# Performance work log

Hardware: AMD Instinct MI355X
Metric: run time of the kernel (lower is better)

The kernel has to match this reference:

```python
import jax, jax.numpy as jnp
import numpy as np

OBS = 4096      # flattened observation size (hardcoded in down_sampler)
ENC = 1024      # encoding_size
LAT = 512       # policy_latent_size
ACT = 3         # action_space_n
B = 4096        # batch
NMAX = 8        # max neighbors (padded ragged dim)


def setup_inputs() -> dict:
    key = jax.random.key(0)
    ks = jax.random.split(key, 16)

    def w(i, shape, fan_in):
        return jax.random.normal(ks[i], shape, jnp.float32) * (1.0 / np.sqrt(fan_in))

    return {
        "observation": jax.random.normal(ks[0], (B, OBS), jnp.float32),
        "neighbors": jax.random.normal(ks[1], (B, NMAX, LAT), jnp.float32),
        "neighbor_counts": jax.random.randint(ks[2], (B,), 0, 9, jnp.int32),
        # down_sampler: Linear(4096, ENC) + ReLU
        "W_ds": w(3, (ENC, OBS), OBS), "b_ds": jnp.zeros((ENC,), jnp.float32),
        # policy: Linear(ENC, LAT) + ReLU
        "W_pol": w(4, (LAT, ENC), ENC), "b_pol": jnp.zeros((LAT,), jnp.float32),
        # v_net: Linear(ENC, 1) + Tanh
        "W_v": w(5, (1, ENC), ENC), "b_v": jnp.zeros((1,), jnp.float32),
        # GRUCell(LAT, LAT): weight_ih [3L, L], weight_hh [3L, L]
        "W_ih": w(6, (3 * LAT, LAT), LAT), "b_ih": jnp.zeros((3 * LAT,), jnp.float32),
        "W_hh": w(7, (3 * LAT, LAT), LAT), "b_hh": jnp.zeros((3 * LAT,), jnp.float32),
        # to_probs: Linear(LAT, ACT) + ReLU + Softmax
        "W_pr": w(8, (ACT, LAT), LAT), "b_pr": jnp.zeros((ACT,), jnp.float32),
    }


def _gru_cell(x, h, W_ih, b_ih, W_hh, b_hh):
    # PyTorch GRUCell semantics; gates ordered (r, z, n)
    gi = x @ W_ih.T + b_ih          # [B, 3L]
    gh = h @ W_hh.T + b_hh          # [B, 3L]
    i_r, i_z, i_n = jnp.split(gi, 3, axis=-1)
    h_r, h_z, h_n = jnp.split(gh, 3, axis=-1)
    r = jax.nn.sigmoid(i_r + h_r)
    z = jax.nn.sigmoid(i_z + h_z)
    n = jnp.tanh(i_n + r * h_n)
    return (1.0 - z) * n + z * h


def reference(observation, neighbors, neighbor_counts,
              W_ds, b_ds, W_pol, b_pol, W_v, b_v,
              W_ih, b_ih, W_hh, b_hh, W_pr, b_pr):
    # step 0: forward_initial
    enc = jax.nn.relu(observation @ W_ds.T + b_ds)        # [B, ENC]
    pol = jax.nn.relu(enc @ W_pol.T + b_pol)              # [B, LAT]
    state_vals = jnp.tanh(enc @ W_v.T + b_v)              # [B, 1]

    # step 1: forward_communicate -- ragged GRU recurrence over padded neighbors
    xs = jnp.swapaxes(neighbors, 0, 1)                    # [NMAX, B, LAT]
    ts = jnp.arange(NMAX)

    def step(h, xt):
        x, t = xt
        h_new = _gru_cell(x, h, W_ih, b_ih, W_hh, b_hh)
        valid = (t < neighbor_counts)[:, None]            # mask padded neighbor slots
        return jnp.where(valid, h_new, h), None

    h, _ = jax.lax.scan(step, pol, (xs, ts))              # [B, LAT]

    # step 2: forward_probs
    probs = jax.nn.softmax(jax.nn.relu(h @ W_pr.T + b_pr), axis=-1)  # [B, ACT]
    return probs, state_vals
```

## Files before the change

kernel.cpp:

```cpp
#include <hip/hip_runtime.h>
#include <hip/hip_bf16.h>

typedef __attribute__((ext_vector_type(8))) short short8;
typedef __attribute__((ext_vector_type(4))) float floatx4;

__device__ __forceinline__ ushort f2bf(float x) {
    unsigned u = __float_as_uint(x);
    unsigned r = (u + 0x7fffu + ((u >> 16) & 1u)) >> 16;
    return (ushort)r;
}
__device__ __forceinline__ float bf2f(ushort h) {
    return __uint_as_float(((unsigned)h) << 16);
}
__device__ __forceinline__ float fast_sigmoid(float x) {
    return 1.0f / (1.0f + __expf(-x));
}
__device__ __forceinline__ float fast_tanh(float x) {
    x = fminf(fmaxf(x, -15.0f), 15.0f);
    float e = __expf(2.0f * x);
    return (e - 1.0f) / (e + 1.0f);
}
__device__ __forceinline__ void load_lds16(const void* g, void* l) {
    __builtin_amdgcn_global_load_lds(
        (__attribute__((address_space(1))) void*)(g),
        (__attribute__((address_space(3))) void*)(l),
        16, 0, 0);
}

__device__ __forceinline__ void stage_unit(const ushort* grow0, int ld, ushort* lds_unit) {
    const int lane = threadIdx.x & 63;
    const int r = lane >> 3;
    const int c = (lane & 7) ^ r;
    load_lds16(grow0 + (size_t)r * ld + c * 8, lds_unit);
}
__device__ __forceinline__ short8 lds_read8(const ushort* buf, int R, int c_el) {
    const int idx = ((R >> 3) << 9) + ((R & 7) << 6) + ((((c_el >> 3) ^ (R & 7))) << 3);
    return *(const short8*)(buf + idx);
}

__global__ __launch_bounds__(256) void cvt_f32_bf16(const float* __restrict__ src,
                                                    ushort* __restrict__ dst, int n4) {
    int i = blockIdx.x * blockDim.x + threadIdx.x;
    if (i >= n4) return;
    const float4 v = ((const float4*)src)[i];
    ushort4 o;
    o.x = f2bf(v.x); o.y = f2bf(v.y); o.z = f2bf(v.z); o.w = f2bf(v.w);
    ((ushort4*)dst)[i] = o;
}

template <int MODE, int BN, int KSPLIT>
__global__ __launch_bounds__(256, 2) void gemm64(
    const ushort* __restrict__ A, int lda,
    const ushort* __restrict__ B, int ldb,
    const float* __restrict__ bias,
    ushort* __restrict__ Cb, float* __restrict__ Cf, int ldc,
    int K, size_t part_stride) {
    __shared__ __attribute__((aligned(16))) ushort sA[64 * 64];
    __shared__ __attribute__((aligned(16))) ushort sB[BN * 64];

    constexpr int NJ = BN / 64;
    constexpr int UB = BN / 32;

    const int tid = threadIdx.x;
    const int lane = tid & 63;
    const int w = tid >> 6;
    const int m0 = blockIdx.y * 64;
    const int n0 = blockIdx.x * BN;
    const int wn = w * (16 * NJ);
    const int nl = lane & 15;

    const int Kper = K / KSPLIT;
    const int kbase = (KSPLIT > 1) ? blockIdx.z * Kper : 0;
    if (MODE == 3) Cf += (size_t)blockIdx.z * part_stride;

    floatx4 acc[4][NJ] = {};

    for (int k0 = kbase; k0 < kbase + Kper; k0 += 64) {
#pragma unroll
        for (int u = 0; u < 2; ++u) {
            const int ua = w * 2 + u;
            stage_unit(A + (size_t)(m0 + ua * 8) * lda + k0, lda, &sA[ua * 512]);
        }
#pragma unroll
        for (int u = 0; u < UB; ++u) {
            const int ub = w * UB + u;
            stage_unit(B + (size_t)(n0 + ub * 8) * ldb + k0, ldb, &sB[ub * 512]);
        }
        __syncthreads();
#pragma unroll
        for (int kk = 0; kk < 2; ++kk) {
            const int cb = kk * 32 + (lane >> 4) * 8;
            short8 a[4], b[NJ];
#pragma unroll
            for (int i = 0; i < 4; ++i) a[i] = lds_read8(sA, i * 16 + nl, cb);
#pragma unroll
            for (int j = 0; j < NJ; ++j) b[j] = lds_read8(sB, wn + j * 16 + nl, cb);
#pragma unroll
            for (int i = 0; i < 4; ++i)
#pragma unroll
                for (int j = 0; j < NJ; ++j)
                    acc[i][j] = __builtin_amdgcn_mfma_f32_16x16x32_bf16(a[i], b[j], acc[i][j], 0, 0, 0);
        }
        __syncthreads();
    }

    const int ml = (lane >> 4) * 4;
#pragma unroll
    for (int j = 0; j < NJ; ++j) {
        const int n = n0 + wn + j * 16 + nl;
        float bv = 0.0f;
        if (MODE == 2) bv = bias[n];
#pragma unroll
        for (int i = 0; i < 4; ++i) {
            const int mbase = m0 + i * 16 + ml;
#pragma unroll
            for (int r = 0; r < 4; ++r) {
                float v = acc[i][j][r];
                const size_t off = (size_t)(mbase + r) * ldc + n;
                if (MODE == 2) {
                    v += bv; v = fmaxf(v, 0.0f);
                    Cb[off] = f2bf(v);
                    Cf[off] = v;
                } else {
                    Cf[off] = v;
                }
            }
        }
    }
}

__global__ __launch_bounds__(256) void combine_relu(const float* __restrict__ p0,
                                                    const float* __restrict__ p1,
                                                    const float* __restrict__ bias,
                                                    ushort* __restrict__ ob, int n4) {
    int i = blockIdx.x * blockDim.x + threadIdx.x;
    if (i >= n4) return;
    const float4 a = ((const float4*)p0)[i];
    const float4 b = ((const float4*)p1)[i];
    const int col = (i * 4) & 1023;
    const float4 bs = *(const float4*)(bias + col);
    ushort4 o;
    o.x = f2bf(fmaxf(a.x + b.x + bs.x, 0.f));
    o.y = f2bf(fmaxf(a.y + b.y + bs.y, 0.f));
    o.z = f2bf(fmaxf(a.z + b.z + bs.z, 0.f));
    o.w = f2bf(fmaxf(a.w + b.w + bs.w, 0.f));
    ((ushort4*)ob)[i] = o;
}

__global__ __launch_bounds__(256, 2) void gru_step(
    const ushort* __restrict__ X,
    const ushort* __restrict__ Hin,
    const ushort* __restrict__ Wih,
    const ushort* __restrict__ Whh,
    const float* __restrict__ bih, const float* __restrict__ bhh,
    const int* __restrict__ cnt,
    float* __restrict__ hf, ushort* __restrict__ Hout, int t) {
    __shared__ __attribute__((aligned(16))) ushort sX[64 * 64];
    __shared__ __attribute__((aligned(16))) ushort sH[64 * 64];
    __shared__ __attribute__((aligned(16))) ushort sBih[192 * 64];
    __shared__ __attribute__((aligned(16))) ushort sBhh[192 * 64];
    __shared__ int scnt[64];

    const int tid = threadIdx.x;
    const int lane = tid & 63;
    const int w = tid >> 6;
    const int s = blockIdx.x;
    const int m0 = blockIdx.y * 64;

    if (tid < 64) scnt[tid] = cnt[m0 + tid];

    const int nl = lane & 15;
    const int ml = (lane >> 4) * 4;
    const int col = s * 64 + w * 16 + nl;

    floatx4 accr[4], accz[4], accn[4], acch[4];
    {
        const float br_ = bih[col] + bhh[col];
        const float bz_ = bih[512 + col] + bhh[512 + col];
        const float bn_i = bih[1024 + col];
        const float bn_h = bhh[1024 + col];
        const floatx4 vr = {br_, br_, br_, br_};
        const floatx4 vz = {bz_, bz_, bz_, bz_};
        const floatx4 vi = {bn_i, bn_i, bn_i, bn_i};
        const floatx4 vh = {bn_h, bn_h, bn_h, bn_h};
#pragma unroll
        for (int i = 0; i < 4; ++i) { accr[i] = vr; accz[i] = vz; accn[i] = vi; acch[i] = vh; }
    }

    for (int k0 = 0; k0 < 512; k0 += 64) {
#pragma unroll
        for (int u = 0; u < 2; ++u) {
            const int ua = w * 2 + u;
            stage_unit(X + (size_t)(m0 + ua * 8) * 4096 + k0, 4096, &sX[ua * 512]);
            stage_unit(Hin + (size_t)(m0 + ua * 8) * 512 + k0, 512, &sH[ua * 512]);
        }
#pragma unroll
        for (int j = 0; j < 6; ++j) {
            const int u = w * 6 + j;
            const int grow0 = (u >> 3) * 512 + s * 64 + (u & 7) * 8;
            stage_unit(Wih + (size_t)grow0 * 512 + k0, 512, &sBih[u * 512]);
            stage_unit(Whh + (size_t)grow0 * 512 + k0, 512, &sBhh[u * 512]);
        }
        __syncthreads();
#pragma unroll
        for (int kk = 0; kk < 2; ++kk) {
            const int cb = kk * 32 + (lane >> 4) * 8;
            short8 ax[4], ah[4];
#pragma unroll
            for (int i = 0; i < 4; ++i) {
                ax[i] = lds_read8(sX, i * 16 + nl, cb);
                ah[i] = lds_read8(sH, i * 16 + nl, cb);
            }
            const short8 bir = lds_read8(sBih, w * 16 + nl, cb);
            const short8 biz = lds_read8(sBih, 64 + w * 16 + nl, cb);
            const short8 bin = lds_read8(sBih, 128 + w * 16 + nl, cb);
            const short8 bhr = lds_read8(sBhh, w * 16 + nl, cb);
            const short8 bhz = lds_read8(sBhh, 64 + w * 16 + nl, cb);
            const short8 bhn = lds_read8(sBhh, 128 + w * 16 + nl, cb);
#pragma unroll
            for (int i = 0; i < 4; ++i) {
                accr[i] = __builtin_amdgcn_mfma_f32_16x16x32_bf16(ax[i], bir, accr[i], 0, 0, 0);
                accr[i] = __builtin_amdgcn_mfma_f32_16x16x32_bf16(ah[i], bhr, accr[i], 0, 0, 0);
                accz[i] = __builtin_amdgcn_mfma_f32_16x16x32_bf16(ax[i], biz, accz[i], 0, 0, 0);
                accz[i] = __builtin_amdgcn_mfma_f32_16x16x32_bf16(ah[i], bhz, accz[i], 0, 0, 0);
                accn[i] = __builtin_amdgcn_mfma_f32_16x16x32_bf16(ax[i], bin, accn[i], 0, 0, 0);
                acch[i] = __builtin_amdgcn_mfma_f32_16x16x32_bf16(ah[i], bhn, acch[i], 0, 0, 0);
            }
        }
        __syncthreads();
    }

#pragma unroll
    for (int i = 0; i < 4; ++i) {
#pragma unroll
        for (int r = 0; r < 4; ++r) {
            const int lr = i * 16 + ml + r;
            const int row = m0 + lr;
            const float rg = fast_sigmoid(accr[i][r]);
            const float zg = fast_sigmoid(accz[i][r]);
            const float ng = fast_tanh(accn[i][r] + rg * acch[i][r]);
            const size_t off = (size_t)row * 512 + col;
            const float ho = hf[off];
            const float hv = (t < scnt[lr]) ? ((1.0f - zg) * ng + zg * ho) : ho;
            hf[off] = hv;
            Hout[off] = f2bf(hv);
        }
    }
}

__global__ __launch_bounds__(256) void v_kernel(const ushort* __restrict__ enc,
                                                const float* __restrict__ Wv,
                                                const float* __restrict__ bv,
                                                float* __restrict__ out) {
    const int row = blockIdx.x * 4 + (threadIdx.x >> 6);
    const int lane = threadIdx.x & 63;
    const ushort* e = enc + (size_t)row * 1024;
    float s = 0.0f;
#pragma unroll
    for (int i = 0; i < 16; ++i) {
        int k = lane + i * 64;
        s += bf2f(e[k]) * Wv[k];
    }
#pragma unroll
    for (int off = 32; off; off >>= 1) s += __shfl_down(s, off, 64);
    if (lane == 0) out[row] = fast_tanh(s + bv[0]);
}

__global__ __launch_bounds__(256) void probs_kernel(const float* __restrict__ h,
                                                    const float* __restrict__ Wpr,
                                                    const float* __restrict__ bpr,
                                                    float* __restrict__ out) {
    const int row = blockIdx.x * 4 + (threadIdx.x >> 6);
    const int lane = threadIdx.x & 63;
    const float* hr = h + (size_t)row * 512;
    float p0 = 0.f, p1 = 0.f, p2 = 0.f;
#pragma unroll
    for (int i = 0; i < 8; ++i) {
        int k = lane + i * 64;
        float x = hr[k];
        p0 += x * Wpr[k];
        p1 += x * Wpr[512 + k];
        p2 += x * Wpr[1024 + k];
    }
#pragma unroll
    for (int off = 32; off; off >>= 1) {
        p0 += __shfl_down(p0, off, 64);
        p1 += __shfl_down(p1, off, 64);
        p2 += __shfl_down(p2, off, 64);
    }
    if (lane == 0) {
        p0 = fmaxf(p0 + bpr[0], 0.f);
        p1 = fmaxf(p1 + bpr[1], 0.f);
        p2 = fmaxf(p2 + bpr[2], 0.f);
        float m = fmaxf(p0, fmaxf(p1, p2));
        float e0 = __expf(p0 - m), e1 = __expf(p1 - m), e2 = __expf(p2 - m);
        float inv = 1.0f / (e0 + e1 + e2);
        out[row * 3 + 0] = e0 * inv;
        out[row * 3 + 1] = e1 * inv;
        out[row * 3 + 2] = e2 * inv;
    }
}

extern "C" void kernel_launch(void* const* d_in, const int* in_sizes, int n_in,
                              void* d_out, int out_size, void* d_ws, size_t ws_size,
                              hipStream_t stream) {
    const float* obs   = (const float*)d_in[0];
    const float* nbr   = (const float*)d_in[1];
    const int*   cnt   = (const int*)d_in[2];
    const float* W_ds  = (const float*)d_in[3];
    const float* b_ds  = (const float*)d_in[4];
    const float* W_pol = (const float*)d_in[5];
    const float* b_pol = (const float*)d_in[6];
    const float* W_v   = (const float*)d_in[7];
    const float* b_v   = (const float*)d_in[8];
    const float* W_ih  = (const float*)d_in[9];
    const float* b_ih  = (const float*)d_in[10];
    const float* W_hh  = (const float*)d_in[11];
    const float* b_hh  = (const float*)d_in[12];
    const float* W_pr  = (const float*)d_in[13];
    const float* b_pr  = (const float*)d_in[14];
    float* out = (float*)d_out;

    ushort* obs_b  = (ushort*)d_ws;
    ushort* nbr_b  = obs_b + 16777216;
    ushort* Wds_b  = nbr_b + 16777216;
    ushort* Wpol_b = Wds_b + 4194304;
    ushort* Wih_b  = Wpol_b + 524288;
    ushort* Whh_b  = Wih_b + 786432;
    ushort* enc_b  = Whh_b + 786432;
    ushort* h_b0   = enc_b + 4194304;
    ushort* h_b1   = h_b0 + 2097152;
    float*  h_f    = (float*)(h_b1 + 2097152);
    float*  part   = h_f + 2097152;

    cvt_f32_bf16<<<16384, 256, 0, stream>>>(obs, obs_b, 4194304);
    cvt_f32_bf16<<<16384, 256, 0, stream>>>(nbr, nbr_b, 4194304);
    cvt_f32_bf16<<<4096, 256, 0, stream>>>(W_ds, Wds_b, 1048576);
    cvt_f32_bf16<<<512, 256, 0, stream>>>(W_pol, Wpol_b, 131072);
    cvt_f32_bf16<<<768, 256, 0, stream>>>(W_ih, Wih_b, 196608);
    cvt_f32_bf16<<<768, 256, 0, stream>>>(W_hh, Whh_b, 196608);

    gemm64<3, 256, 2><<<dim3(4, 64, 2), 256, 0, stream>>>(
        obs_b, 4096, Wds_b, 4096, nullptr, nullptr, part, 1024, 4096, 4194304);
    combine_relu<<<4096, 256, 0, stream>>>(part, part + 4194304, b_ds, enc_b, 1048576);

    gemm64<2, 128, 1><<<dim3(4, 64, 1), 256, 0, stream>>>(
        enc_b, 1024, Wpol_b, 1024, b_pol, h_b0, h_f, 512, 1024, 0);

    v_kernel<<<1024, 256, 0, stream>>>(enc_b, W_v, b_v, out + 12288);

    for (int t = 0; t < 8; ++t) {
        const ushort* hin = (t & 1) ? h_b1 : h_b0;
        ushort* hout = (t & 1) ? h_b0 : h_b1;
        gru_step<<<dim3(8, 64), 256, 0, stream>>>(nbr_b + t * 512, hin, Wih_b, Whh_b,
                                                  b_ih, b_hh, cnt, h_f, hout, t);
    }

    probs_kernel<<<1024, 256, 0, stream>>>(h_f, W_pr, b_pr, out);
}
```

Baseline: 463.4 us.

## Sort batch rows by neighbor count and skip inactive GRU tiles

```diff
diff --git a/kernel.cpp b/kernel.cpp
--- a/kernel.cpp
+++ b/kernel.cpp
@@ -48,17 +48,47 @@
     ((ushort4*)dst)[i] = o;
 }
 
-template <int MODE, int BN, int KSPLIT>
+__global__ __launch_bounds__(256) void sort_by_cnt(const int* __restrict__ cnt,
+                                                   int* __restrict__ perm,
+                                                   int* __restrict__ inv,
+                                                   int* __restrict__ nact) {
+    __shared__ int h[9];
+    __shared__ int cur[9];
+    const int tid = threadIdx.x;
+    if (tid < 9) h[tid] = 0;
+    __syncthreads();
+    for (int i = tid; i < 4096; i += 256) atomicAdd(&h[cnt[i]], 1);
+    __syncthreads();
+    if (tid == 0) {
+        int off = 0;
+        for (int c = 8; c >= 0; --c) { cur[c] = off; off += h[c]; }
+        for (int t = 0; t < 8; ++t) {
+            int n = 0;
+            for (int c = t + 1; c <= 8; ++c) n += h[c];
+            nact[t] = n;
+        }
+    }
+    __syncthreads();
+    for (int i = tid; i < 4096; i += 256) {
+        const int c = cnt[i];
+        const int p = atomicAdd(&cur[c], 1);
+        perm[p] = i;
+        inv[i] = p;
+    }
+}
+
+template <int MODE, int BN, int KSPLIT, bool MAP>
 __global__ __launch_bounds__(256, 2) void gemm64(
     const ushort* __restrict__ A, int lda,
     const ushort* __restrict__ B, int ldb,
     const float* __restrict__ bias,
+    const int* __restrict__ row_map,
     ushort* __restrict__ Cb, float* __restrict__ Cf, int ldc,
     int K, size_t part_stride) {
     __shared__ __attribute__((aligned(16))) ushort sA[64 * 64];
     __shared__ __attribute__((aligned(16))) ushort sB[BN * 64];
 
-    constexpr int NJ = BN / 64;
+    constexpr int NJ = (BN + 63) / 64;
     constexpr int UB = BN / 32;
 
     const int tid = threadIdx.x;
@@ -116,7 +146,9 @@
 #pragma unroll
             for (int r = 0; r < 4; ++r) {
                 float v = acc[i][j][r];
-                const size_t off = (size_t)(mbase + r) * ldc + n;
+                const int mr = mbase + r;
+                const int orow = MAP ? row_map[mr] : mr;
+                const size_t off = (size_t)orow * ldc + n;
                 if (MODE == 2) {
                     v += bv; v = fmaxf(v, 0.0f);
                     Cb[off] = f2bf(v);
@@ -148,30 +180,61 @@
 }
 
 __global__ __launch_bounds__(256, 2) void gru_step(
-    const ushort* __restrict__ X,
+    const ushort* __restrict__ Xall,
     const ushort* __restrict__ Hin,
     const ushort* __restrict__ Wih,
     const ushort* __restrict__ Whh,
     const float* __restrict__ bih, const float* __restrict__ bhh,
-    const int* __restrict__ cnt,
+    const int* __restrict__ perm, const int* __restrict__ nact,
     float* __restrict__ hf, ushort* __restrict__ Hout, int t) {
     __shared__ __attribute__((aligned(16))) ushort sX[64 * 64];
     __shared__ __attribute__((aligned(16))) ushort sH[64 * 64];
     __shared__ __attribute__((aligned(16))) ushort sBih[192 * 64];
     __shared__ __attribute__((aligned(16))) ushort sBhh[192 * 64];
-    __shared__ int scnt[64];
 
     const int tid = threadIdx.x;
     const int lane = tid & 63;
     const int w = tid >> 6;
     const int s = blockIdx.x;
     const int m0 = blockIdx.y * 64;
-
-    if (tid < 64) scnt[tid] = cnt[m0 + tid];
+    const int na = nact[t];
+
+    if (m0 >= na) {
+        const int rr = tid >> 2;
+        const size_t base = (size_t)(m0 + rr) * 512 + s * 64;
+        const uint4* src = (const uint4*)(Hin + base);
+        uint4* dst = (uint4*)(Hout + base);
+        const int cc = (tid & 3) * 2;
+        dst[cc] = src[cc];
+        dst[cc + 1] = src[cc + 1];
+        return;
+    }
 
     const int nl = lane & 15;
     const int ml = (lane >> 4) * 4;
     const int col = s * 64 + w * 16 + nl;
+
+    const int r = lane >> 3;
+    const int c = (lane & 7) ^ r;
+    const ushort* X = Xall + t * 512;
+    const ushort* xb[2];
+    const ushort* hbp[2];
+#pragma unroll
+    for (int u = 0; u < 2; ++u) {
+        const int srow = m0 + (w * 2 + u) * 8 + r;
+        const int orig = perm[srow];
+        xb[u] = X + (size_t)orig * 4096 + c * 8;
+        hbp[u] = Hin + (size_t)srow * 512 + c * 8;
+    }
+    const ushort* wi[6];
+    const ushort* wh[6];
+#pragma unroll
+    for (int j = 0; j < 6; ++j) {
+        const int u = w * 6 + j;
+        const int grow = (u >> 3) * 512 + s * 64 + (u & 7) * 8 + r;
+        wi[j] = Wih + (size_t)grow * 512 + c * 8;
+        wh[j] = Whh + (size_t)grow * 512 + c * 8;
+    }
 
     floatx4 accr[4], accz[4], accn[4], acch[4];
     {
@@ -191,15 +254,14 @@
 #pragma unroll
         for (int u = 0; u < 2; ++u) {
             const int ua = w * 2 + u;
-            stage_unit(X + (size_t)(m0 + ua * 8) * 4096 + k0, 4096, &sX[ua * 512]);
-            stage_unit(Hin + (size_t)(m0 + ua * 8) * 512 + k0, 512, &sH[ua * 512]);
+            load_lds16(xb[u] + k0, &sX[ua * 512]);
+            load_lds16(hbp[u] + k0, &sH[ua * 512]);
         }
 #pragma unroll
         for (int j = 0; j < 6; ++j) {
             const int u = w * 6 + j;
-            const int grow0 = (u >> 3) * 512 + s * 64 + (u & 7) * 8;
-            stage_unit(Wih + (size_t)grow0 * 512 + k0, 512, &sBih[u * 512]);
-            stage_unit(Whh + (size_t)grow0 * 512 + k0, 512, &sBhh[u * 512]);
+            load_lds16(wi[j] + k0, &sBih[u * 512]);
+            load_lds16(wh[j] + k0, &sBhh[u * 512]);
         }
         __syncthreads();
 #pragma unroll
@@ -230,18 +292,20 @@
         __syncthreads();
     }
 
+    const bool full = (m0 + 64 <= na);
 #pragma unroll
     for (int i = 0; i < 4; ++i) {
 #pragma unroll
-        for (int r = 0; r < 4; ++r) {
-            const int lr = i * 16 + ml + r;
+        for (int r4 = 0; r4 < 4; ++r4) {
+            const int lr = i * 16 + ml + r4;
             const int row = m0 + lr;
-            const float rg = fast_sigmoid(accr[i][r]);
-            const float zg = fast_sigmoid(accz[i][r]);
-            const float ng = fast_tanh(accn[i][r] + rg * acch[i][r]);
+            const float rg = fast_sigmoid(accr[i][r4]);
+            const float zg = fast_sigmoid(accz[i][r4]);
+            const float ng = fast_tanh(accn[i][r4] + rg * acch[i][r4]);
             const size_t off = (size_t)row * 512 + col;
             const float ho = hf[off];
-            const float hv = (t < scnt[lr]) ? ((1.0f - zg) * ng + zg * ho) : ho;
+            const bool act = full || (row < na);
+            const float hv = act ? ((1.0f - zg) * ng + zg * ho) : ho;
             hf[off] = hv;
             Hout[off] = f2bf(hv);
         }
@@ -269,10 +333,11 @@
 __global__ __launch_bounds__(256) void probs_kernel(const float* __restrict__ h,
                                                     const float* __restrict__ Wpr,
                                                     const float* __restrict__ bpr,
+                                                    const int* __restrict__ perm,
                                                     float* __restrict__ out) {
-    const int row = blockIdx.x * 4 + (threadIdx.x >> 6);
+    const int srow = blockIdx.x * 4 + (threadIdx.x >> 6);
     const int lane = threadIdx.x & 63;
-    const float* hr = h + (size_t)row * 512;
+    const float* hr = h + (size_t)srow * 512;
     float p0 = 0.f, p1 = 0.f, p2 = 0.f;
 #pragma unroll
     for (int i = 0; i < 8; ++i) {
@@ -289,15 +354,16 @@
         p2 += __shfl_down(p2, off, 64);
     }
     if (lane == 0) {
+        const int orow = perm[srow];
         p0 = fmaxf(p0 + bpr[0], 0.f);
         p1 = fmaxf(p1 + bpr[1], 0.f);
         p2 = fmaxf(p2 + bpr[2], 0.f);
         float m = fmaxf(p0, fmaxf(p1, p2));
         float e0 = __expf(p0 - m), e1 = __expf(p1 - m), e2 = __expf(p2 - m);
         float inv = 1.0f / (e0 + e1 + e2);
-        out[row * 3 + 0] = e0 * inv;
-        out[row * 3 + 1] = e1 * inv;
-        out[row * 3 + 2] = e2 * inv;
+        out[orow * 3 + 0] = e0 * inv;
+        out[orow * 3 + 1] = e1 * inv;
+        out[orow * 3 + 2] = e2 * inv;
     }
 }
 
@@ -322,8 +388,7 @@
     float* out = (float*)d_out;
 
     ushort* obs_b  = (ushort*)d_ws;
-    ushort* nbr_b  = obs_b + 16777216;
-    ushort* Wds_b  = nbr_b + 16777216;
+    ushort* Wds_b  = obs_b + 16777216;
     ushort* Wpol_b = Wds_b + 4194304;
     ushort* Wih_b  = Wpol_b + 524288;
     ushort* Whh_b  = Wih_b + 786432;
@@ -332,29 +397,36 @@
     ushort* h_b1   = h_b0 + 2097152;
     float*  h_f    = (float*)(h_b1 + 2097152);
     float*  part   = h_f + 2097152;
+    ushort* nbr_b  = (ushort*)part;
+    int*    perm   = (int*)(part + 8388608);
+    int*    inv    = perm + 4096;
+    int*    nact   = inv + 4096;
+
+    sort_by_cnt<<<1, 256, 0, stream>>>(cnt, perm, inv, nact);
 
     cvt_f32_bf16<<<16384, 256, 0, stream>>>(obs, obs_b, 4194304);
-    cvt_f32_bf16<<<16384, 256, 0, stream>>>(nbr, nbr_b, 4194304);
     cvt_f32_bf16<<<4096, 256, 0, stream>>>(W_ds, Wds_b, 1048576);
     cvt_f32_bf16<<<512, 256, 0, stream>>>(W_pol, Wpol_b, 131072);
     cvt_f32_bf16<<<768, 256, 0, stream>>>(W_ih, Wih_b, 196608);
     cvt_f32_bf16<<<768, 256, 0, stream>>>(W_hh, Whh_b, 196608);
 
-    gemm64<3, 256, 2><<<dim3(4, 64, 2), 256, 0, stream>>>(
-        obs_b, 4096, Wds_b, 4096, nullptr, nullptr, part, 1024, 4096, 4194304);
+    gemm64<3, 128, 2, false><<<dim3(8, 64, 2), 256, 0, stream>>>(
+        obs_b, 4096, Wds_b, 4096, nullptr, nullptr, nullptr, part, 1024, 4096, 4194304);
     combine_relu<<<4096, 256, 0, stream>>>(part, part + 4194304, b_ds, enc_b, 1048576);
 
-    gemm64<2, 128, 1><<<dim3(4, 64, 1), 256, 0, stream>>>(
-        enc_b, 1024, Wpol_b, 1024, b_pol, h_b0, h_f, 512, 1024, 0);
+    cvt_f32_bf16<<<16384, 256, 0, stream>>>(nbr, nbr_b, 4194304);
+
+    gemm64<2, 64, 1, true><<<dim3(8, 64, 1), 256, 0, stream>>>(
+        enc_b, 1024, Wpol_b, 1024, b_pol, inv, h_b0, h_f, 512, 1024, 0);
 
     v_kernel<<<1024, 256, 0, stream>>>(enc_b, W_v, b_v, out + 12288);
 
     for (int t = 0; t < 8; ++t) {
         const ushort* hin = (t & 1) ? h_b1 : h_b0;
         ushort* hout = (t & 1) ? h_b0 : h_b1;
-        gru_step<<<dim3(8, 64), 256, 0, stream>>>(nbr_b + t * 512, hin, Wih_b, Whh_b,
-                                                  b_ih, b_hh, cnt, h_f, hout, t);
-    }
-
-    probs_kernel<<<1024, 256, 0, stream>>>(h_f, W_pr, b_pr, out);
-}
+        gru_step<<<dim3(8, 64), 256, 0, stream>>>(nbr_b, hin, Wih_b, Whh_b,
+                                                  b_ih, b_hh, perm, nact, h_f, hout, t);
+    }
+
+    probs_kernel<<<1024, 256, 0, stream>>>(h_f, W_pr, b_pr, perm, out);
+}
```

Measured after the change: 445.6 us. -3.9%, faster.
